# Kernel optimization log

Measured on AMD Instinct MI355X. Metric: run time of the kernel, lower is better.

Reference implementation:

```python
import jax, jax.numpy as jnp
import numpy as np

N, D, H, E, TOP_K = 32768, 768, 256, 8, 2


def setup_inputs() -> dict:
    key = jax.random.key(0)
    ks = jax.random.split(key, 9)
    s_in = 1.0 / np.sqrt(D)
    s_hid = 1.0 / np.sqrt(H)
    return {
        "x": jax.random.normal(ks[0], (N, D), dtype=jnp.float32),
        # per-expert MLP weights, stacked over expert dim E
        "W1": jax.random.uniform(ks[1], (E, D, H), jnp.float32, -s_in, s_in),
        "b1": jax.random.uniform(ks[2], (E, H), jnp.float32, -s_in, s_in),
        "W2": jax.random.uniform(ks[3], (E, H, D), jnp.float32, -s_hid, s_hid),
        "b2": jax.random.uniform(ks[4], (E, D), jnp.float32, -s_hid, s_hid),
        # gate MLP: Linear(D,H) -> ReLU -> Linear(H,E)
        "Wg1": jax.random.uniform(ks[5], (D, H), jnp.float32, -s_in, s_in),
        "bg1": jax.random.uniform(ks[6], (H,), jnp.float32, -s_in, s_in),
        "Wg2": jax.random.uniform(ks[7], (H, E), jnp.float32, -s_hid, s_hid),
        "bg2": jax.random.uniform(ks[8], (E,), jnp.float32, -s_hid, s_hid),
    }


def reference(x, W1, b1, W2, b2, Wg1, bg1, Wg2, bg2):
    # gating
    gate_scores = jax.nn.relu(x @ Wg1 + bg1) @ Wg2 + bg2          # [N, E]
    gate_probs = jax.nn.softmax(gate_scores, axis=-1)              # [N, E]
    top_k_probs, top_k_idx = jax.lax.top_k(gate_probs, TOP_K)      # [N, K]
    top_k_probs = top_k_probs / jnp.sum(top_k_probs, axis=-1, keepdims=True)

    # dense all-expert compute (faithful to original: every expert on every token)
    h = jax.nn.relu(jnp.einsum("nd,edh->enh", x, W1) + b1[:, None, :])  # [E, N, H]
    expert_out = jnp.einsum("enh,ehd->end", h, W2) + b2[:, None, :]      # [E, N, D]

    # gather selected experts per token and combine
    tok = jnp.arange(x.shape[0])[:, None]                          # [N, 1]
    sel = expert_out[top_k_idx, tok, :]                            # [N, K, D]
    output = jnp.sum(top_k_probs[..., None] * sel, axis=1)          # [N, D]
    return output, gate_probs
```

## Files before the change

### kernel.cpp

```cpp
#include <hip/hip_runtime.h>
#include <hip/hip_bf16.h>
#include <stdint.h>

#define NTOK 32768
#define DIM  768
#define HID  256
#define NEXP 8
#define PADC 144

typedef float f32x4 __attribute__((ext_vector_type(4)));
typedef short s16x8 __attribute__((ext_vector_type(8)));

__device__ __forceinline__ unsigned short f2bf(float f) {
  union { float f; unsigned int u; } c; c.f = f;
  unsigned int r = c.u + 0x7fffu + ((c.u >> 16) & 1u);
  return (unsigned short)(r >> 16);
}

__device__ __forceinline__ float bf2f(unsigned int u) {
  union { unsigned int x; float f; } c; c.x = u << 16; return c.f;
}

__device__ __forceinline__ unsigned short f2h(float f) {
  union { _Float16 h; unsigned short u; } c; c.h = (_Float16)f; return c.u;
}

__device__ __forceinline__ float h2f(unsigned short u) {
  union { unsigned short u; _Float16 h; } c; c.u = u; return (float)c.h;
}

__device__ __forceinline__ void gload_lds16(const unsigned short* g, unsigned short* l) {
  __builtin_amdgcn_global_load_lds((const __attribute__((address_space(1))) void*)g,
                                   (__attribute__((address_space(3))) void*)l, 16, 0, 0);
}

__global__ __launch_bounds__(256) void k_cvt_x(const float* __restrict__ x,
                                               unsigned short* __restrict__ xf16) {
  int i = (blockIdx.x * 256 + threadIdx.x) * 8;
  float4 a = *(const float4*)(x + i);
  float4 b = *(const float4*)(x + i + 4);
  float f[8] = {a.x, a.y, a.z, a.w, b.x, b.y, b.z, b.w};
  unsigned short hh[8];
#pragma unroll
  for (int q = 0; q < 8; ++q) hh[q] = f2h(f[q]);
  int4 vh;
  vh.x = (int)((unsigned)hh[0] | ((unsigned)hh[1] << 16));
  vh.y = (int)((unsigned)hh[2] | ((unsigned)hh[3] << 16));
  vh.z = (int)((unsigned)hh[4] | ((unsigned)hh[5] << 16));
  vh.w = (int)((unsigned)hh[6] | ((unsigned)hh[7] << 16));
  *(int4*)(xf16 + i) = vh;
}

__global__ __launch_bounds__(256) void k_trh(const float* __restrict__ in,
                                             unsigned short* __restrict__ outp,
                                             int R, int C) {
  __shared__ float tile[32][33];
  int e = blockIdx.z;
  const float* ip = in + (size_t)e * R * C;
  unsigned short* op = outp + (size_t)e * R * C;
  int tx = threadIdx.x & 31, ty = threadIdx.x >> 5;
  int r0 = blockIdx.y * 32, c0 = blockIdx.x * 32;
#pragma unroll
  for (int i = 0; i < 4; ++i)
    tile[ty + i * 8][tx] = ip[(size_t)(r0 + ty + i * 8) * C + c0 + tx];
  __syncthreads();
#pragma unroll
  for (int i = 0; i < 4; ++i)
    op[(size_t)(c0 + ty + i * 8) * R + r0 + tx] = f2h(tile[tx][ty + i * 8]);
}

__global__ __launch_bounds__(256) void k_gmfma(const unsigned short* __restrict__ xh,
                                               const unsigned short* __restrict__ wh,
                                               const float* __restrict__ bg1,
                                               unsigned short* __restrict__ hg) {
  int bm = blockIdx.x * 128;
  int bn = blockIdx.y * 128;

  __shared__ __align__(16) unsigned short Ah[128 * 64];
  __shared__ __align__(16) unsigned short Bh[128 * 64];

  int tid = threadIdx.x;
  int lane = tid & 63;
  int wid = tid >> 6;
  int wm = wid >> 1, wn = wid & 1;
  int ar = lane & 15, kg = lane >> 4;

  const unsigned short *sah[4], *sbh[4];
  unsigned short *dA[4], *dB[4];
#pragma unroll
  for (int i = 0; i < 4; ++i) {
    int cb0 = i * 256 + wid * 64;
    int ci = cb0 + lane;
    int row = ci >> 3;
    int cb = (ci & 7) ^ (row & 7);
    sah[i] = xh + (size_t)(bm + row) * DIM + cb * 8;
    sbh[i] = wh + (size_t)(bn + row) * DIM + cb * 8;
    dA[i] = &Ah[cb0 * 8];
    dB[i] = &Bh[cb0 * 8];
  }

  f32x4 acc[4][4] = {};

  for (int kt = 0; kt < DIM / 64; ++kt) {
#pragma unroll
    for (int i = 0; i < 4; ++i) {
      gload_lds16(sah[i] + kt * 64, dA[i]);
      gload_lds16(sbh[i] + kt * 64, dB[i]);
    }
    __syncthreads();
#pragma unroll
    for (int ks = 0; ks < 2; ++ks) {
      int kc = ks * 4 + kg;
      s16x8 a[4], b[4];
#pragma unroll
      for (int m = 0; m < 4; ++m) {
        int row = wm * 64 + m * 16 + ar;
        a[m] = *(const s16x8*)&Ah[row * 64 + ((kc ^ (row & 7)) * 8)];
      }
#pragma unroll
      for (int n = 0; n < 4; ++n) {
        int row = wn * 64 + n * 16 + ar;
        b[n] = *(const s16x8*)&Bh[row * 64 + ((kc ^ (row & 7)) * 8)];
      }
#pragma unroll
      for (int m = 0; m < 4; ++m)
#pragma unroll
        for (int n = 0; n < 4; ++n)
          acc[m][n] = __builtin_amdgcn_mfma_f32_16x16x32_f16(a[m], b[n], acc[m][n], 0, 0, 0);
    }
    __syncthreads();
  }

#pragma unroll
  for (int n = 0; n < 4; ++n) {
    int col = bn + wn * 64 + n * 16 + ar;
    float bb = bg1[col];
#pragma unroll
    for (int m = 0; m < 4; ++m) {
      int rbase = bm + wm * 64 + m * 16 + kg * 4;
#pragma unroll
      for (int r = 0; r < 4; ++r)
        hg[(size_t)(rbase + r) * HID + col] = f2h(fmaxf(acc[m][n][r] + bb, 0.f));
    }
  }
}

__global__ __launch_bounds__(256) void k_gate2a(const unsigned short* __restrict__ hg,
                                                const float* __restrict__ wg2,
                                                const float* __restrict__ bg2,
                                                float* __restrict__ gs,
                                                int* __restrict__ rcnt,
                                                int* __restrict__ rlist) {
  int tok = blockIdx.x * 256 + threadIdx.x;
  const unsigned short* hrow = hg + (size_t)tok * HID;

  float s[8];
#pragma unroll
  for (int e = 0; e < 8; ++e) s[e] = bg2[e];
#pragma unroll 4
  for (int j = 0; j < 32; ++j) {
    s16x8 hv8 = *(const s16x8*)(hrow + j * 8);
#pragma unroll
    for (int i = 0; i < 8; ++i) {
      float hv = h2f((unsigned short)hv8[i]);
      const float* wr = wg2 + (j * 8 + i) * 8;
#pragma unroll
      for (int e = 0; e < 8; ++e) s[e] += hv * wr[e];
    }
  }

  f32x4 o0 = {s[0], s[1], s[2], s[3]};
  f32x4 o1 = {s[4], s[5], s[6], s[7]};
  *(f32x4*)&gs[(size_t)tok * 8] = o0;
  *(f32x4*)&gs[(size_t)tok * 8 + 4] = o1;

  float m1 = -3e38f, m2 = -3e38f, m3 = -3e38f;
#pragma unroll
  for (int e = 0; e < 8; ++e) {
    float v = s[e];
    if (v > m1)      { m3 = m2; m2 = m1; m1 = v; }
    else if (v > m2) { m3 = m2; m2 = v; }
    else if (v > m3) { m3 = v; }
  }
  if (m2 - m3 < 1e-3f) {
    int i = atomicAdd(rcnt, 1);
    rlist[i] = tok;
  }
}

__global__ __launch_bounds__(256) void k_rescue(const float* __restrict__ x,
                                                const float* __restrict__ wg1,
                                                const float* __restrict__ bg1,
                                                const float* __restrict__ wg2,
                                                const float* __restrict__ bg2,
                                                const int* __restrict__ rcnt,
                                                const int* __restrict__ rlist,
                                                float* __restrict__ gs) {
  __shared__ float xs[DIM];
  __shared__ float ps[4][8];
  int n = rcnt[0];
  int tid = threadIdx.x;
  int lane = tid & 63, wid = tid >> 6;
  for (int idx = blockIdx.x; idx < n; idx += 2048) {
    int tok = rlist[idx];
    __syncthreads();
#pragma unroll
    for (int q = 0; q < 3; ++q) xs[tid + q * 256] = x[(size_t)tok * DIM + tid + q * 256];
    __syncthreads();
    const float* wcol = wg1 + tid;
    float pa[8] = {};
#pragma unroll 4
    for (int k0 = 0; k0 < DIM; k0 += 8) {
#pragma unroll
      for (int q = 0; q < 8; ++q)
        pa[q] = fmaf(xs[k0 + q], wcol[(size_t)(k0 + q) * HID], pa[q]);
    }
    float acc = bg1[tid] +
                (((pa[0] + pa[1]) + (pa[2] + pa[3])) + ((pa[4] + pa[5]) + (pa[6] + pa[7])));
    float hj = fmaxf(acc, 0.f);
    float p[8];
#pragma unroll
    for (int e = 0; e < 8; ++e) p[e] = hj * wg2[tid * 8 + e];
#pragma unroll
    for (int off = 32; off >= 1; off >>= 1) {
#pragma unroll
      for (int e = 0; e < 8; ++e) p[e] += __shfl_xor(p[e], off);
    }
    if (lane == 0) {
#pragma unroll
      for (int e = 0; e < 8; ++e) ps[wid][e] = p[e];
    }
    __syncthreads();
    if (tid < 8)
      gs[(size_t)tok * 8 + tid] = bg2[tid] + ps[0][tid] + ps[1][tid] + ps[2][tid] + ps[3][tid];
  }
}

__global__ __launch_bounds__(256) void k_gate2b(const float* __restrict__ gs,
                                                float* __restrict__ gprob,
                                                int* __restrict__ cnt,
                                                int* __restrict__ lists,
                                                float* __restrict__ wts) {
  __shared__ int lcnt[8];
  __shared__ int sbase[8];
  __shared__ int se1[256], se2[256], sp1[256], sp2[256];
  __shared__ float sw1[256], sw2[256];
  int tid = threadIdx.x;
  if (tid < 8) lcnt[tid] = 0;
  __syncthreads();

  int tok = blockIdx.x * 256 + tid;
  f32x4 s0v = *(const f32x4*)&gs[(size_t)tok * 8];
  f32x4 s1v = *(const f32x4*)&gs[(size_t)tok * 8 + 4];
  float s[8] = {s0v[0], s0v[1], s0v[2], s0v[3], s1v[0], s1v[1], s1v[2], s1v[3]};

  float m = s[0];
#pragma unroll
  for (int e = 1; e < 8; ++e) m = fmaxf(m, s[e]);
  float p[8]; float sum = 0.f;
#pragma unroll
  for (int e = 0; e < 8; ++e) { p[e] = expf(s[e] - m); sum += p[e]; }
  float inv = 1.f / sum;
#pragma unroll
  for (int e = 0; e < 8; ++e) p[e] *= inv;

  f32x4 o0 = {p[0], p[1], p[2], p[3]};
  f32x4 o1 = {p[4], p[5], p[6], p[7]};
  *(f32x4*)&gprob[(size_t)tok * 8] = o0;
  *(f32x4*)&gprob[(size_t)tok * 8 + 4] = o1;

  int e1 = 0; float p1 = p[0];
#pragma unroll
  for (int e = 1; e < 8; ++e) if (p[e] > p1) { p1 = p[e]; e1 = e; }
  int e2 = -1; float p2 = -1.f;
#pragma unroll
  for (int e = 0; e < 8; ++e) if (e != e1 && p[e] > p2) { p2 = p[e]; e2 = e; }
  float rinv = 1.f / (p1 + p2);

  int pos1 = atomicAdd(&lcnt[e1], 1);
  int pos2 = atomicAdd(&lcnt[e2], 1);
  se1[tid] = e1; sp1[tid] = pos1; sw1[tid] = p1 * rinv;
  se2[tid] = e2; sp2[tid] = pos2; sw2[tid] = p2 * rinv;
  __syncthreads();

  if (tid < 8) sbase[tid] = atomicAdd(&cnt[tid * 32], lcnt[tid]);
  __syncthreads();

  int a1i = sbase[se1[tid]] + sp1[tid];
  lists[se1[tid] * NTOK + a1i] = tok; wts[se1[tid] * NTOK + a1i] = sw1[tid];
  int a2i = sbase[se2[tid]] + sp2[tid];
  lists[se2[tid] * NTOK + a2i] = tok; wts[se2[tid] * NTOK + a2i] = -sw2[tid];
}

__global__ __launch_bounds__(512) void k_ffn1(const unsigned short* __restrict__ xf16,
                                              const unsigned short* __restrict__ w1t,
                                              const float* __restrict__ b1,
                                              const int* __restrict__ cnt,
                                              const int* __restrict__ lists,
                                              unsigned short* __restrict__ h) {
  int id = blockIdx.x;
  int xcd = id & 7, local = id >> 3;
  int xh = local & 31, e = local >> 5;
  int row0 = ((xh << 3) | xcd) * 128;

  int c = cnt[e * 32];
  if (row0 >= c) return;
  int pfx = 0;
#pragma unroll
  for (int j = 0; j < 8; ++j) if (j < e) pfx += cnt[j * 32];

  __shared__ __align__(16) unsigned short smem[(1024 + 2048) * 8];
  __shared__ int stok[128];

  int tid = threadIdx.x;
  int lane = tid & 63;
  int wid = tid >> 6;
  int wm = wid >> 2, wn = wid & 3;
  int ar = lane & 15, kg = lane >> 4;

  if (tid < 128) stok[tid] = lists[e * NTOK + min(row0 + tid, c - 1)];
  __syncthreads();

  const unsigned short* asrc[2];
  unsigned short* ldsA[2];
#pragma unroll
  for (int q = 0; q < 2; ++q) {
    int cb0 = q * 512 + wid * 64;
    int ci = cb0 + lane;
    int row = ci >> 3;
    int cb = (ci & 7) ^ (row & 7);
    asrc[q] = xf16 + (size_t)stok[row] * DIM + cb * 8;
    ldsA[q] = &smem[cb0 * 8];
  }
  const unsigned short* bsrc[4];
  unsigned short* ldsB[4];
#pragma unroll
  for (int q = 0; q < 4; ++q) {
    int cb0 = q * 512 + wid * 64;
    int ci = cb0 + lane;
    int row = ci >> 3;
    int cb = (ci & 7) ^ (row & 7);
    bsrc[q] = w1t + ((size_t)e * HID + row) * DIM + cb * 8;
    ldsB[q] = &smem[8192 + cb0 * 8];
  }

  f32x4 acc[4][4] = {};

  for (int kt = 0; kt < DIM / 64; ++kt) {
#pragma unroll
    for (int q = 0; q < 2; ++q) gload_lds16(asrc[q] + kt * 64, ldsA[q]);
#pragma unroll
    for (int q = 0; q < 4; ++q) gload_lds16(bsrc[q] + kt * 64, ldsB[q]);
    __syncthreads();
#pragma unroll
    for (int ks = 0; ks < 2; ++ks) {
      int kc = ks * 4 + kg;
      s16x8 a[4], b[4];
#pragma unroll
      for (int m = 0; m < 4; ++m) {
        int row = wm * 64 + m * 16 + ar;
        a[m] = *(const s16x8*)&smem[row * 64 + ((kc ^ (row & 7)) * 8)];
      }
#pragma unroll
      for (int n = 0; n < 4; ++n) {
        int row = wn * 64 + n * 16 + ar;
        b[n] = *(const s16x8*)&smem[8192 + row * 64 + ((kc ^ (row & 7)) * 8)];
      }
#pragma unroll
      for (int m = 0; m < 4; ++m)
#pragma unroll
        for (int n = 0; n < 4; ++n)
          acc[m][n] = __builtin_amdgcn_mfma_f32_16x16x32_f16(a[m], b[n], acc[m][n], 0, 0, 0);
    }
    __syncthreads();
  }

  int hbase = pfx + row0;
#pragma unroll 1
  for (int half = 0; half < 2; ++half) {
    if ((wn >> 1) == half) {
#pragma unroll
      for (int n = 0; n < 4; ++n) {
        int col = (wn & 1) * 64 + n * 16 + ar;
        float bb = b1[e * HID + half * 128 + col];
#pragma unroll
        for (int m = 0; m < 4; ++m) {
          int rloc = wm * 64 + m * 16 + kg * 4;
#pragma unroll
          for (int r = 0; r < 4; ++r)
            smem[(rloc + r) * PADC + col] = f2h(fmaxf(acc[m][n][r] + bb, 0.f));
        }
      }
    }
    __syncthreads();
#pragma unroll
    for (int q = 0; q < 4; ++q) {
      int ci = tid + q * 512;
      int row = ci >> 4, ch = ci & 15;
      if (row0 + row < c) {
        int4 v = *(const int4*)&smem[row * PADC + ch * 8];
        *(int4*)&h[(size_t)(hbase + row) * HID + half * 128 + ch * 8] = v;
      }
    }
    __syncthreads();
  }
}

template <bool STORE_PART>
__global__ __launch_bounds__(256) void k_ffn2(const unsigned short* __restrict__ h,
                                              const unsigned short* __restrict__ w2t,
                                              const float* __restrict__ b2,
                                              const int* __restrict__ cnt,
                                              const int* __restrict__ lists,
                                              const float* __restrict__ wts,
                                              unsigned short* __restrict__ part0,
                                              unsigned short* __restrict__ part1,
                                              float* __restrict__ out) {
  int id = blockIdx.x;
  int xcd = id & 7, local = id >> 3;
  int bny = local % 6;
  int r2 = local / 6;
  int xh = r2 & 31, e = r2 >> 5;
  int row0 = ((xh << 3) | xcd) * 128;
  int bn = bny * 128;

  int c = cnt[e * 32];
  if (row0 >= c) return;
  int pfx = 0;
#pragma unroll
  for (int j = 0; j < 8; ++j) if (j < e) pfx += cnt[j * 32];

  __shared__ __align__(16) unsigned short smem[128 * PADC];
  __shared__ int stok[128];
  __shared__ float swt[128];
  unsigned short* As = smem;
  unsigned short* Bs = smem + 128 * 64;

  int tid = threadIdx.x;
  int lane = tid & 63;
  int wid = tid >> 6;
  int wm = wid >> 1, wn = wid & 1;
  int ar = lane & 15, kg = lane >> 4;

  if (tid < 128) {
    int r = row0 + tid;
    stok[tid] = (r < c) ? lists[e * NTOK + r] : 0;
    swt[tid]  = (r < c) ? wts[e * NTOK + r] : 0.f;
  }
  __syncthreads();

  const unsigned short* asrc[4];
  const unsigned short* bsrc[4];
  unsigned short* ldsA[4];
  unsigned short* ldsB[4];
#pragma unroll
  for (int i = 0; i < 4; ++i) {
    int cb0 = i * 256 + wid * 64;
    int ci = cb0 + lane;
    int row = ci >> 3;
    int cb = (ci & 7) ^ (row & 7);
    asrc[i] = h + (size_t)(pfx + row0 + row) * HID + cb * 8;
    bsrc[i] = w2t + ((size_t)e * DIM + bn + row) * HID + cb * 8;
    ldsA[i] = &As[cb0 * 8];
    ldsB[i] = &Bs[cb0 * 8];
  }

  f32x4 acc[4][4] = {};

  for (int kt = 0; kt < HID / 64; ++kt) {
#pragma unroll
    for (int i = 0; i < 4; ++i) {
      gload_lds16(asrc[i] + kt * 64, ldsA[i]);
      gload_lds16(bsrc[i] + kt * 64, ldsB[i]);
    }
    __syncthreads();
#pragma unroll
    for (int ks = 0; ks < 2; ++ks) {
      int kc = ks * 4 + kg;
      s16x8 a[4], b[4];
#pragma unroll
      for (int m = 0; m < 4; ++m) {
        int row = wm * 64 + m * 16 + ar;
        a[m] = *(const s16x8*)&As[row * 64 + ((kc ^ (row & 7)) * 8)];
      }
#pragma unroll
      for (int n = 0; n < 4; ++n) {
        int row = wn * 64 + n * 16 + ar;
        b[n] = *(const s16x8*)&Bs[row * 64 + ((kc ^ (row & 7)) * 8)];
      }
#pragma unroll
      for (int m = 0; m < 4; ++m)
#pragma unroll
        for (int n = 0; n < 4; ++n)
          acc[m][n] = __builtin_amdgcn_mfma_f32_16x16x32_f16(a[m], b[n], acc[m][n], 0, 0, 0);
    }
    __syncthreads();
  }

  if constexpr (STORE_PART) {
#pragma unroll
    for (int n = 0; n < 4; ++n) {
      int col = wn * 64 + n * 16 + ar;
      float bb = b2[e * DIM + bn + col];
#pragma unroll
      for (int m = 0; m < 4; ++m) {
        int rloc = wm * 64 + m * 16 + kg * 4;
#pragma unroll
        for (int r = 0; r < 4; ++r) {
          float w = swt[rloc + r];
          smem[(rloc + r) * PADC + col] = f2bf((acc[m][n][r] + bb) * fabsf(w));
        }
      }
    }
    __syncthreads();
#pragma unroll
    for (int q = 0; q < 8; ++q) {
      int ci = tid + q * 256;
      int row = ci >> 4, ch = ci & 15;
      float w = swt[row];
      if (w != 0.f) {
        unsigned short* dst = (w > 0.f) ? part0 : part1;
        int4 v = *(const int4*)&smem[row * PADC + ch * 8];
        *(int4*)&dst[(size_t)stok[row] * DIM + bn + ch * 8] = v;
      }
    }
  } else {
#pragma unroll
    for (int n = 0; n < 4; ++n) {
      int col = bn + wn * 64 + n * 16 + ar;
      float bb = b2[e * DIM + col];
#pragma unroll
      for (int m = 0; m < 4; ++m) {
        int rloc = wm * 64 + m * 16 + kg * 4;
#pragma unroll
        for (int r = 0; r < 4; ++r) {
          float w = swt[rloc + r];
          if (w != 0.f) {
            float v = (acc[m][n][r] + bb) * fabsf(w);
            atomicAdd(&out[(size_t)stok[rloc + r] * DIM + col], v);
          }
        }
      }
    }
  }
}

__global__ __launch_bounds__(256) void k_combine(const unsigned short* __restrict__ p0,
                                                 const unsigned short* __restrict__ p1,
                                                 float* __restrict__ out) {
  size_t i = ((size_t)blockIdx.x * 256 + threadIdx.x) * 8;
  int4 a = *(const int4*)(p0 + i);
  int4 b = *(const int4*)(p1 + i);
  unsigned int ua[4] = {(unsigned)a.x, (unsigned)a.y, (unsigned)a.z, (unsigned)a.w};
  unsigned int ub[4] = {(unsigned)b.x, (unsigned)b.y, (unsigned)b.z, (unsigned)b.w};
  float o[8];
#pragma unroll
  for (int q = 0; q < 4; ++q) {
    o[q * 2 + 0] = bf2f(ua[q] & 0xffffu) + bf2f(ub[q] & 0xffffu);
    o[q * 2 + 1] = bf2f(ua[q] >> 16)     + bf2f(ub[q] >> 16);
  }
  *(float4*)(out + i)     = *(float4*)&o[0];
  *(float4*)(out + i + 4) = *(float4*)&o[4];
}

extern "C" void kernel_launch(void* const* d_in, const int* in_sizes, int n_in,
                              void* d_out, int out_size, void* d_ws, size_t ws_size,
                              hipStream_t stream) {
  const float* x   = (const float*)d_in[0];
  const float* W1  = (const float*)d_in[1];
  const float* b1  = (const float*)d_in[2];
  const float* W2  = (const float*)d_in[3];
  const float* b2  = (const float*)d_in[4];
  const float* Wg1 = (const float*)d_in[5];
  const float* bg1 = (const float*)d_in[6];
  const float* Wg2 = (const float*)d_in[7];
  const float* bg2 = (const float*)d_in[8];
  float* out = (float*)d_out;
  float* gprob = out + (size_t)NTOK * DIM;

  char* ws = (char*)d_ws;
  size_t off = 0;
  auto alloc = [&](size_t bytes) { void* pp = ws + off; off += (bytes + 255) & ~(size_t)255; return pp; };
  unsigned short* w1t = (unsigned short*)alloc((size_t)NEXP * HID * DIM * 2);
  unsigned short* w2t = (unsigned short*)alloc((size_t)NEXP * DIM * HID * 2);
  float* hgbuf = (float*)alloc((size_t)NTOK * HID * 4);
  int* cnt = (int*)alloc(NEXP * 32 * 4);
  int* lists = (int*)alloc((size_t)NEXP * NTOK * 4);
  float* wts = (float*)alloc((size_t)NEXP * NTOK * 4);
  unsigned short* part0 = (unsigned short*)alloc((size_t)NTOK * DIM * 2);
  unsigned short* part1 = (unsigned short*)alloc((size_t)NTOK * DIM * 2);
  bool store_mode = (off <= ws_size);

  unsigned short *xf16, *wg1t;
  float* gs; int* rcnt; int* rlist;
  if (store_mode) {
    xf16 = part1;
    wg1t = part0;
    char* p0b = (char*)part0;
    gs    = (float*)(p0b + (1u << 20));
    rcnt  = (int*)(p0b + 9 * (1u << 18));
    rlist = (int*)(p0b + 10 * (1u << 18));
  } else {
    xf16  = (unsigned short*)alloc((size_t)NTOK * DIM * 2);
    wg1t  = (unsigned short*)alloc((size_t)DIM * HID * 2);
    gs    = (float*)alloc((size_t)NTOK * 8 * 4);
    rcnt  = (int*)alloc(256);
    rlist = (int*)alloc((size_t)NTOK * 4);
  }

  unsigned short* hg = (unsigned short*)hgbuf;
  unsigned short* h = (unsigned short*)hgbuf;

  hipMemsetAsync(cnt, 0, NEXP * 32 * sizeof(int), stream);
  hipMemsetAsync(rcnt, 0, sizeof(int), stream);
  if (!store_mode)
    hipMemsetAsync(d_out, 0, (size_t)NTOK * DIM * sizeof(float), stream);

  k_cvt_x<<<(NTOK * DIM) / (256 * 8), 256, 0, stream>>>(x, xf16);
  k_trh<<<dim3(HID / 32, DIM / 32, 1), 256, 0, stream>>>(Wg1, wg1t, DIM, HID);
  k_trh<<<dim3(HID / 32, DIM / 32, NEXP), 256, 0, stream>>>(W1, w1t, DIM, HID);
  k_trh<<<dim3(DIM / 32, HID / 32, NEXP), 256, 0, stream>>>(W2, w2t, HID, DIM);
  k_gmfma<<<dim3(NTOK / 128, HID / 128), 256, 0, stream>>>(xf16, wg1t, bg1, hg);
  k_gate2a<<<NTOK / 256, 256, 0, stream>>>(hg, Wg2, bg2, gs, rcnt, rlist);
  k_rescue<<<2048, 256, 0, stream>>>(x, Wg1, bg1, Wg2, bg2, rcnt, rlist, gs);
  k_gate2b<<<NTOK / 256, 256, 0, stream>>>(gs, gprob, cnt, lists, wts);
  k_ffn1<<<(NTOK / 128) * NEXP, 512, 0, stream>>>(xf16, w1t, b1, cnt, lists, h);
  if (store_mode) {
    k_ffn2<true><<<(NTOK / 128) * 6 * NEXP, 256, 0, stream>>>(h, w2t, b2, cnt, lists, wts, part0, part1, out);
    k_combine<<<(NTOK * DIM) / (256 * 8), 256, 0, stream>>>(part0, part1, out);
  } else {
    k_ffn2<false><<<(NTOK / 128) * 6 * NEXP, 256, 0, stream>>>(h, w2t, b2, cnt, lists, wts, part0, part1, out);
  }
}
```

Before: 240.7 us.

## Fuse gate first GEMM with second gate layer and merge weight transposes

The gate's first GEMM now covers the full hidden width per 128-token block with 512 threads, and the ReLU activations stay in shared memory. A per-block reduction against Wg2 then produces the gate scores and flags near-tie tokens in the same kernel. This removes the round trip of the hidden gate activations through global memory and one kernel launch. Separately, the W1 and Wg1 transposes are merged into one launch. The trade-offs are larger shared-memory use, half as many blocks for the GEMM, and extra synchronisation inside the fused kernel.

```diff
diff --git a/kernel.cpp b/kernel.cpp
--- a/kernel.cpp
+++ b/kernel.cpp
@@ -69,122 +69,156 @@
     op[(size_t)(c0 + ty + i * 8) * R + r0 + tx] = f2h(tile[tx][ty + i * 8]);
 }
 
-__global__ __launch_bounds__(256) void k_gmfma(const unsigned short* __restrict__ xh,
-                                               const unsigned short* __restrict__ wh,
-                                               const float* __restrict__ bg1,
-                                               unsigned short* __restrict__ hg) {
-  int bm = blockIdx.x * 128;
-  int bn = blockIdx.y * 128;
-
-  __shared__ __align__(16) unsigned short Ah[128 * 64];
-  __shared__ __align__(16) unsigned short Bh[128 * 64];
-
-  int tid = threadIdx.x;
-  int lane = tid & 63;
-  int wid = tid >> 6;
-  int wm = wid >> 1, wn = wid & 1;
-  int ar = lane & 15, kg = lane >> 4;
-
-  const unsigned short *sah[4], *sbh[4];
-  unsigned short *dA[4], *dB[4];
-#pragma unroll
-  for (int i = 0; i < 4; ++i) {
-    int cb0 = i * 256 + wid * 64;
-    int ci = cb0 + lane;
-    int row = ci >> 3;
-    int cb = (ci & 7) ^ (row & 7);
-    sah[i] = xh + (size_t)(bm + row) * DIM + cb * 8;
-    sbh[i] = wh + (size_t)(bn + row) * DIM + cb * 8;
-    dA[i] = &Ah[cb0 * 8];
-    dB[i] = &Bh[cb0 * 8];
-  }
-
-  f32x4 acc[4][4] = {};
-
-  for (int kt = 0; kt < DIM / 64; ++kt) {
-#pragma unroll
-    for (int i = 0; i < 4; ++i) {
-      gload_lds16(sah[i] + kt * 64, dA[i]);
-      gload_lds16(sbh[i] + kt * 64, dB[i]);
-    }
-    __syncthreads();
-#pragma unroll
-    for (int ks = 0; ks < 2; ++ks) {
-      int kc = ks * 4 + kg;
-      s16x8 a[4], b[4];
-#pragma unroll
-      for (int m = 0; m < 4; ++m) {
-        int row = wm * 64 + m * 16 + ar;
-        a[m] = *(const s16x8*)&Ah[row * 64 + ((kc ^ (row & 7)) * 8)];
-      }
-#pragma unroll
-      for (int n = 0; n < 4; ++n) {
-        int row = wn * 64 + n * 16 + ar;
-        b[n] = *(const s16x8*)&Bh[row * 64 + ((kc ^ (row & 7)) * 8)];
-      }
-#pragma unroll
-      for (int m = 0; m < 4; ++m)
-#pragma unroll
-        for (int n = 0; n < 4; ++n)
-          acc[m][n] = __builtin_amdgcn_mfma_f32_16x16x32_f16(a[m], b[n], acc[m][n], 0, 0, 0);
-    }
-    __syncthreads();
-  }
-
-#pragma unroll
-  for (int n = 0; n < 4; ++n) {
-    int col = bn + wn * 64 + n * 16 + ar;
-    float bb = bg1[col];
-#pragma unroll
-    for (int m = 0; m < 4; ++m) {
-      int rbase = bm + wm * 64 + m * 16 + kg * 4;
-#pragma unroll
-      for (int r = 0; r < 4; ++r)
-        hg[(size_t)(rbase + r) * HID + col] = f2h(fmaxf(acc[m][n][r] + bb, 0.f));
-    }
-  }
-}
-
-__global__ __launch_bounds__(256) void k_gate2a(const unsigned short* __restrict__ hg,
+__global__ __launch_bounds__(256) void k_trh9(const float* __restrict__ W1,
+                                              const float* __restrict__ Wg1,
+                                              unsigned short* __restrict__ w1t,
+                                              unsigned short* __restrict__ wg1t) {
+  __shared__ float tile[32][33];
+  int z = blockIdx.z;
+  const float* ip = (z < 8) ? W1 + (size_t)z * DIM * HID : Wg1;
+  unsigned short* op = (z < 8) ? w1t + (size_t)z * DIM * HID : wg1t;
+  int tx = threadIdx.x & 31, ty = threadIdx.x >> 5;
+  int r0 = blockIdx.y * 32, c0 = blockIdx.x * 32;
+#pragma unroll
+  for (int i = 0; i < 4; ++i)
+    tile[ty + i * 8][tx] = ip[(size_t)(r0 + ty + i * 8) * HID + c0 + tx];
+  __syncthreads();
+#pragma unroll
+  for (int i = 0; i < 4; ++i)
+    op[(size_t)(c0 + ty + i * 8) * DIM + r0 + tx] = f2h(tile[tx][ty + i * 8]);
+}
+
+__global__ __launch_bounds__(512) void k_gate1f(const unsigned short* __restrict__ xf16,
+                                                const unsigned short* __restrict__ wg1t,
+                                                const float* __restrict__ bg1,
                                                 const float* __restrict__ wg2,
                                                 const float* __restrict__ bg2,
                                                 float* __restrict__ gs,
                                                 int* __restrict__ rcnt,
                                                 int* __restrict__ rlist) {
-  int tok = blockIdx.x * 256 + threadIdx.x;
-  const unsigned short* hrow = hg + (size_t)tok * HID;
-
-  float s[8];
-#pragma unroll
-  for (int e = 0; e < 8; ++e) s[e] = bg2[e];
-#pragma unroll 4
-  for (int j = 0; j < 32; ++j) {
-    s16x8 hv8 = *(const s16x8*)(hrow + j * 8);
-#pragma unroll
-    for (int i = 0; i < 8; ++i) {
-      float hv = h2f((unsigned short)hv8[i]);
-      const float* wr = wg2 + (j * 8 + i) * 8;
-#pragma unroll
-      for (int e = 0; e < 8; ++e) s[e] += hv * wr[e];
-    }
-  }
-
-  f32x4 o0 = {s[0], s[1], s[2], s[3]};
-  f32x4 o1 = {s[4], s[5], s[6], s[7]};
-  *(f32x4*)&gs[(size_t)tok * 8] = o0;
-  *(f32x4*)&gs[(size_t)tok * 8 + 4] = o1;
-
-  float m1 = -3e38f, m2 = -3e38f, m3 = -3e38f;
-#pragma unroll
-  for (int e = 0; e < 8; ++e) {
-    float v = s[e];
-    if (v > m1)      { m3 = m2; m2 = m1; m1 = v; }
-    else if (v > m2) { m3 = m2; m2 = v; }
-    else if (v > m3) { m3 = v; }
-  }
-  if (m2 - m3 < 1e-3f) {
-    int i = atomicAdd(rcnt, 1);
-    rlist[i] = tok;
+  int bm = blockIdx.x * 128;
+
+  __shared__ __align__(16) unsigned short smem[(1024 + 2048) * 8];
+  unsigned short* hs = smem;
+  float* sc = (float*)&smem[16896];
+  float* wg2s = (float*)&smem[20480];
+
+  int tid = threadIdx.x;
+  int lane = tid & 63;
+  int wid = tid >> 6;
+  int wm = wid >> 2, wn = wid & 3;
+  int ar = lane & 15, kg = lane >> 4;
+
+  const unsigned short* asrc[2];
+  unsigned short* ldsA[2];
+#pragma unroll
+  for (int q = 0; q < 2; ++q) {
+    int cb0 = q * 512 + wid * 64;
+    int ci = cb0 + lane;
+    int row = ci >> 3;
+    int cb = (ci & 7) ^ (row & 7);
+    asrc[q] = xf16 + (size_t)(bm + row) * DIM + cb * 8;
+    ldsA[q] = &smem[cb0 * 8];
+  }
+  const unsigned short* bsrc[4];
+  unsigned short* ldsB[4];
+#pragma unroll
+  for (int q = 0; q < 4; ++q) {
+    int cb0 = q * 512 + wid * 64;
+    int ci = cb0 + lane;
+    int row = ci >> 3;
+    int cb = (ci & 7) ^ (row & 7);
+    bsrc[q] = wg1t + (size_t)row * DIM + cb * 8;
+    ldsB[q] = &smem[8192 + cb0 * 8];
+  }
+
+  f32x4 acc[4][4] = {};
+
+  for (int kt = 0; kt < DIM / 64; ++kt) {
+#pragma unroll
+    for (int q = 0; q < 2; ++q) gload_lds16(asrc[q] + kt * 64, ldsA[q]);
+#pragma unroll
+    for (int q = 0; q < 4; ++q) gload_lds16(bsrc[q] + kt * 64, ldsB[q]);
+    __syncthreads();
+#pragma unroll
+    for (int ks = 0; ks < 2; ++ks) {
+      int kc = ks * 4 + kg;
+      s16x8 a[4], b[4];
+#pragma unroll
+      for (int m = 0; m < 4; ++m) {
+        int row = wm * 64 + m * 16 + ar;
+        a[m] = *(const s16x8*)&smem[row * 64 + ((kc ^ (row & 7)) * 8)];
+      }
+#pragma unroll
+      for (int n = 0; n < 4; ++n) {
+        int row = wn * 64 + n * 16 + ar;
+        b[n] = *(const s16x8*)&smem[8192 + row * 64 + ((kc ^ (row & 7)) * 8)];
+      }
+#pragma unroll
+      for (int m = 0; m < 4; ++m)
+#pragma unroll
+        for (int n = 0; n < 4; ++n)
+          acc[m][n] = __builtin_amdgcn_mfma_f32_16x16x32_f16(a[m], b[n], acc[m][n], 0, 0, 0);
+    }
+    __syncthreads();
+  }
+
+#pragma unroll
+  for (int j = 0; j < 4; ++j) wg2s[tid * 4 + j] = wg2[tid * 4 + j];
+
+  int tok2 = (tid & 63) * 2;
+  int ex = tid >> 6;
+  float s0 = 0.f, s1 = 0.f;
+#pragma unroll 1
+  for (int half = 0; half < 2; ++half) {
+    if ((wn >> 1) == half) {
+#pragma unroll
+      for (int n = 0; n < 4; ++n) {
+        int col = (wn & 1) * 64 + n * 16 + ar;
+        float bb = bg1[half * 128 + col];
+#pragma unroll
+        for (int m = 0; m < 4; ++m) {
+          int rbase = wm * 64 + m * 16 + kg * 4;
+#pragma unroll
+          for (int r = 0; r < 4; ++r)
+            hs[col * 132 + rbase + r] = f2h(fmaxf(acc[m][n][r] + bb, 0.f));
+        }
+      }
+    }
+    __syncthreads();
+#pragma unroll 8
+    for (int c = 0; c < 128; ++c) {
+      unsigned int pair = *(const unsigned int*)&hs[c * 132 + tok2];
+      float h0 = h2f((unsigned short)(pair & 0xffffu));
+      float h1 = h2f((unsigned short)(pair >> 16));
+      float w = wg2s[(half * 128 + c) * 8 + ex];
+      s0 = fmaf(h0, w, s0);
+      s1 = fmaf(h1, w, s1);
+    }
+    __syncthreads();
+  }
+
+  float b2e = bg2[ex];
+  s0 += b2e; s1 += b2e;
+  gs[(size_t)(bm + tok2) * 8 + ex] = s0;
+  gs[(size_t)(bm + tok2 + 1) * 8 + ex] = s1;
+  sc[tok2 * 8 + ex] = s0;
+  sc[tok2 * 8 + 8 + ex] = s1;
+  __syncthreads();
+
+  if (tid < 128) {
+    float m1 = -3e38f, m2 = -3e38f, m3 = -3e38f;
+#pragma unroll
+    for (int e = 0; e < 8; ++e) {
+      float v = sc[tid * 8 + e];
+      if (v > m1)      { m3 = m2; m2 = m1; m1 = v; }
+      else if (v > m2) { m3 = m2; m2 = v; }
+      else if (v > m3) { m3 = v; }
+    }
+    if (m2 - m3 < 1e-3f) {
+      int i = atomicAdd(rcnt, 1);
+      rlist[i] = bm + tid;
+    }
   }
 }
 
@@ -608,7 +642,6 @@
     rlist = (int*)alloc((size_t)NTOK * 4);
   }
 
-  unsigned short* hg = (unsigned short*)hgbuf;
   unsigned short* h = (unsigned short*)hgbuf;
 
   hipMemsetAsync(cnt, 0, NEXP * 32 * sizeof(int), stream);
@@ -617,11 +650,9 @@
     hipMemsetAsync(d_out, 0, (size_t)NTOK * DIM * sizeof(float), stream);
 
   k_cvt_x<<<(NTOK * DIM) / (256 * 8), 256, 0, stream>>>(x, xf16);
-  k_trh<<<dim3(HID / 32, DIM / 32, 1), 256, 0, stream>>>(Wg1, wg1t, DIM, HID);
-  k_trh<<<dim3(HID / 32, DIM / 32, NEXP), 256, 0, stream>>>(W1, w1t, DIM, HID);
+  k_trh9<<<dim3(HID / 32, DIM / 32, 9), 256, 0, stream>>>(W1, Wg1, w1t, wg1t);
   k_trh<<<dim3(DIM / 32, HID / 32, NEXP), 256, 0, stream>>>(W2, w2t, HID, DIM);
-  k_gmfma<<<dim3(NTOK / 128, HID / 128), 256, 0, stream>>>(xf16, wg1t, bg1, hg);
-  k_gate2a<<<NTOK / 256, 256, 0, stream>>>(hg, Wg2, bg2, gs, rcnt, rlist);
+  k_gate1f<<<NTOK / 128, 512, 0, stream>>>(xf16, wg1t, bg1, Wg2, bg2, gs, rcnt, rlist);
   k_rescue<<<2048, 256, 0, stream>>>(x, Wg1, bg1, Wg2, bg2, rcnt, rlist, gs);
   k_gate2b<<<NTOK / 256, 256, 0, stream>>>(gs, gprob, cnt, lists, wts);
   k_ffn1<<<(NTOK / 128) * NEXP, 512, 0, stream>>>(xf16, w1t, b1, cnt, lists, h);
```

New measurement: 227.5 us. 1.06x faster.
